# Optimization experiments

Measured on AMD Instinct MI355X. Metric: run time of the kernel, lower is better.

The kernel has to match this reference:

```python
import jax, jax.numpy as jnp
import numpy as np

B, L, D, H, HD = 4, 2048, 1024, 16, 64
SCALE = 1.0 / np.sqrt(HD)
NEG_INF = -1e9


def _apply_rope(x, rope):
    # x: (B, H, L, HD), rope: (L, HD)
    sin = rope[:, ::2]   # (L, HD/2)
    cos = rope[:, 1::2]  # (L, HD/2)
    x_even = x[..., ::2]
    x_odd = x[..., 1::2]
    r_even = x_even * cos - x_odd * sin
    r_odd = x_even * sin + x_odd * cos
    # interleave even/odd back: stack on new last axis then flatten
    return jnp.stack([r_even, r_odd], axis=-1).reshape(x.shape)


def setup_inputs() -> dict:
    key = jax.random.key(0)
    ks = jax.random.split(key, 10)
    s = 0.02
    inp = {
        "q_in": jax.random.normal(ks[0], (B, L, D), jnp.float32),
        "k_in": jax.random.normal(ks[1], (B, L, D), jnp.float32),
        "v_in": jax.random.normal(ks[2], (B, L, D), jnp.float32),
        "mask": jnp.broadcast_to(jnp.tril(jnp.ones((L, L), bool)), (B, L, L)),
        "rope": jax.random.normal(ks[3], (L, HD), jnp.float32),
        "Wq": jax.random.normal(ks[4], (D, H * HD), jnp.float32) * s,
        "bq": jnp.zeros((H * HD,), jnp.float32),
        "Wkv": jax.random.normal(ks[5], (D, 2 * H * HD), jnp.float32) * s,
        "bkv": jnp.zeros((2 * H * HD,), jnp.float32),
        "Wp": jax.random.normal(ks[6], (H * HD, D), jnp.float32) * s,
        "bp": jnp.zeros((D,), jnp.float32),
    }
    return inp


def reference(q_in, k_in, v_in, mask, rope, Wq, bq, Wkv, bkv, Wp, bp):
    q = q_in @ Wq + bq                       # (B, Lq, H*HD)
    kv = k_in @ Wkv + bkv                    # (B, Lk, 2*H*HD)
    k, v = jnp.split(kv, 2, axis=-1)
    q = q.reshape(B, L, H, HD).transpose(0, 2, 1, 3)  # (B, H, Lq, HD)
    k = k.reshape(B, L, H, HD).transpose(0, 2, 1, 3)
    v = v.reshape(B, L, H, HD).transpose(0, 2, 1, 3)
    # rope.shape[0] == Lq == Lk, so both branches fire
    q = _apply_rope(q, rope)
    k = _apply_rope(k, rope)
    logits = jnp.einsum("bhqd,bhkd->bhqk", q, k) * SCALE
    logits = jnp.where(mask[:, None, :, :], logits, NEG_INF)
    attn = jax.nn.softmax(logits, axis=-1)
    out = jnp.einsum("bhqk,bhkd->bhqd", attn, v)
    out = out.transpose(0, 2, 1, 3).reshape(B, L, H * HD)
    return out @ Wp + bp
```

## Files before the change

### kernel.cpp

```cpp
#include <hip/hip_runtime.h>
#include <hip/hip_bf16.h>

typedef __hip_bfloat16 bf16;
typedef short s16x8 __attribute__((ext_vector_type(8)));
typedef float f32x4 __attribute__((ext_vector_type(4)));

#define MFMA16(a, b, c) __builtin_amdgcn_mfma_f32_16x16x32_bf16(a, b, c, 0, 0, 0)
#define SCALE 0.125f

typedef __attribute__((address_space(1))) void gvoid;
typedef __attribute__((address_space(3))) void lvoid;

static __device__ __forceinline__ void lds_cp16(const bf16* g, bf16* l) {
    __builtin_amdgcn_global_load_lds((gvoid*)g, (lvoid*)l, 16, 0, 0);
}

static __device__ __forceinline__ void cast8(const float* __restrict__ src,
                                             bf16* __restrict__ dst, int i) {
    float4 a = *(const float4*)(src + i);
    float4 b = *(const float4*)(src + i + 4);
    bf16 o[8];
    o[0] = __float2bfloat16(a.x); o[1] = __float2bfloat16(a.y);
    o[2] = __float2bfloat16(a.z); o[3] = __float2bfloat16(a.w);
    o[4] = __float2bfloat16(b.x); o[5] = __float2bfloat16(b.y);
    o[6] = __float2bfloat16(b.z); o[7] = __float2bfloat16(b.w);
    *(uint4*)(dst + i) = *(const uint4*)o;
}

__global__ __launch_bounds__(256) void prep(
    const float* __restrict__ q_in, bf16* __restrict__ qbf,
    const float* __restrict__ k_in, bf16* __restrict__ kbf,
    const float* __restrict__ rope, bf16* __restrict__ ropec,
    const float* __restrict__ bq, const float* __restrict__ bkv,
    const float* __restrict__ bp, bf16* __restrict__ bqc,
    bf16* __restrict__ bkvc, bf16* __restrict__ bpc,
    const float* __restrict__ Wq, bf16* __restrict__ WqT,
    const float* __restrict__ Wkv, bf16* __restrict__ WkvT,
    const float* __restrict__ Wp, bf16* __restrict__ WpT) {
    __shared__ bf16 t[32][33];
    const int blk = blockIdx.x;
    const int tid = threadIdx.x;
    if (blk < 8192) {
        int i = (blk * 256 + tid) * 8;
        const float* src;
        bf16* dst;
        if (i < 8388608) {
            src = q_in; dst = qbf;
        } else {
            src = k_in; dst = kbf; i -= 8388608;
        }
        cast8(src, dst, i);
    } else if (blk < 12288) {
        int t2 = blk - 8192;
        int bx = t2 & 127;
        const int y = t2 >> 7;
        const float* in;
        bf16* out;
        int C;
        if (bx < 32) {
            in = Wq; out = WqT; C = 1024;
        } else if (bx < 96) {
            in = Wkv; out = WkvT; C = 2048; bx -= 32;
        } else {
            in = Wp; out = WpT; C = 1024; bx -= 96;
        }
        const int tx = tid & 31, ty = tid >> 5;
        const int c0 = bx * 32, r0 = y * 32;
        for (int i = ty; i < 32; i += 8)
            t[i][tx] = __float2bfloat16(in[(size_t)(r0 + i) * C + c0 + tx]);
        __syncthreads();
        for (int i = ty; i < 32; i += 8)
            out[(size_t)(c0 + i) * 1024 + r0 + tx] = t[tx][i];
    } else if (blk < 12352) {
        int i = ((blk - 12288) * 256 + tid) * 8;
        cast8(rope, ropec, i);
    } else {
        int i = ((blk - 12352) * 256 + tid) * 8;
        const float* src;
        bf16* dst;
        int off;
        if (i < 1024) {
            src = bq; dst = bqc; off = i;
        } else if (i < 3072) {
            src = bkv; dst = bkvc; off = i - 1024;
        } else {
            src = bp; dst = bpc; off = i - 3072;
        }
        cast8(src, dst, off);
    }
}

template <int EPI, int ROPE>
__device__ __forceinline__ void gemm_core(
    const bf16* __restrict__ A, const bf16* __restrict__ BT,
    const bf16* __restrict__ bias, const bf16* __restrict__ ropetab,
    void* __restrict__ out0, bf16* __restrict__ out1, int N, int K, int bx,
    int by, bf16* smA, bf16* smB) {
    const int tid = threadIdx.x;
    const int lane = tid & 63;
    const int wave = tid >> 6;
    const int lm = lane & 15;
    const int lq = lane >> 4;
    const int bm0 = by * 128;
    const int bn0 = bx * 128;
    const int wm = (wave >> 1) * 64;
    const int wn = (wave & 1) * 64;
    const int x7 = lm & 7;

    int srow[4], scol[4], sdst[4];
#pragma unroll
    for (int j = 0; j < 4; ++j) {
        int o = (wave * 4 + j) * 1024 + lane * 16;
        srow[j] = o >> 7;
        scol[j] = (((o >> 4) & 7) ^ (srow[j] & 7)) * 8;
        sdst[j] = (wave * 4 + j) * 512;
    }

    const f32x4 z4 = {0.f, 0.f, 0.f, 0.f};
    f32x4 acc[4][4];
#pragma unroll
    for (int i = 0; i < 4; ++i)
#pragma unroll
        for (int j = 0; j < 4; ++j) acc[i][j] = z4;

    const bf16* gA = A + (size_t)bm0 * K;
    const bf16* gB = BT + (size_t)bn0 * K;
    const int nk = K >> 6;
    for (int kt = 0; kt < nk; ++kt) {
        const size_t ko = (size_t)kt * 64;
#pragma unroll
        for (int j = 0; j < 4; ++j) {
            lds_cp16(gA + (size_t)srow[j] * K + ko + scol[j], smA + sdst[j]);
            lds_cp16(gB + (size_t)srow[j] * K + ko + scol[j], smB + sdst[j]);
        }
        __syncthreads();

#pragma unroll
        for (int kk = 0; kk < 2; ++kk) {
            s16x8 af[4], bfr[4];
#pragma unroll
            for (int i = 0; i < 4; ++i) {
                const int c16 = kk * 4 + lq;
                af[i] = *(const s16x8*)(smA + (wm + i * 16 + lm) * 64 +
                                        ((c16 ^ x7) * 8));
                bfr[i] = *(const s16x8*)(smB + (wn + i * 16 + lm) * 64 +
                                         ((c16 ^ x7) * 8));
            }
            __builtin_amdgcn_s_setprio(1);
#pragma unroll
            for (int i = 0; i < 4; ++i)
#pragma unroll
                for (int j = 0; j < 4; ++j)
                    acc[i][j] = MFMA16(af[i], bfr[j], acc[i][j]);
            __builtin_amdgcn_s_setprio(0);
        }
        __syncthreads();
    }

    if (EPI == 2 && bn0 >= 1024) {
        bf16* T = smA;
#pragma unroll
        for (int j = 0; j < 4; ++j) {
            const int nl = wn + j * 16 + lm;
            const float bv = __bfloat162float(bias[bn0 + nl]);
            const int xsw = (nl & 7) << 3;
#pragma unroll
            for (int i = 0; i < 4; ++i) {
                const int m0 = wm + i * 16 + lq * 4;
                bf16 pk[4];
#pragma unroll
                for (int r = 0; r < 4; ++r)
                    pk[r] = __float2bfloat16(acc[i][j][r] + bv);
                *(uint2*)(T + nl * 128 + (m0 ^ xsw)) = *(const uint2*)pk;
            }
        }
        __syncthreads();
        const int b = bm0 >> 11;
        const int lbase = bm0 & 2047;
#pragma unroll
        for (int p = 0; p < 8; ++p) {
            const int task = p * 256 + tid;
            const int row = task >> 4;
            const int chunk = task & 15;
            const int m8 = chunk * 8;
            uint4 v = *(const uint4*)(T + row * 128 + (m8 ^ ((row & 7) << 3)));
            const int n2 = bn0 - 1024 + row;
            const int h = n2 >> 6, hd = n2 & 63;
            *(uint4*)(out1 + (((size_t)(b * 16 + h) * 64) + hd) * 2048 +
                      lbase + m8) = v;
        }
        return;
    }

#pragma unroll
    for (int j = 0; j < 4; ++j) {
        const int n = bn0 + wn + j * 16 + lm;
        const float bv = __bfloat162float(bias[n]);
#pragma unroll
        for (int i = 0; i < 4; ++i) {
#pragma unroll
            for (int r = 0; r < 4; ++r) {
                const int m = bm0 + wm + i * 16 + lq * 4 + r;
                float v = acc[i][j][r] + bv;
                if (EPI == 0) {
                    ((float*)out0)[(size_t)m * N + n] = v;
                } else {
                    const int b = m >> 11, l = m & 2047;
                    if (ROPE) {
                        float w = __shfl_xor(v, 1, 64);
                        unsigned sc =
                            ((const unsigned*)ropetab)[l * 32 + ((n & 63) >> 1)];
                        float sn = __uint_as_float(sc << 16);
                        float cs = __uint_as_float(sc & 0xffff0000u);
                        v = (n & 1) ? (w * sn + v * cs) : (v * cs - w * sn);
                    }
                    const int h = (n & 1023) >> 6, hd = n & 63;
                    ((bf16*)out0)[(((size_t)(b * 16 + h) * 2048) + l) * 64 +
                                  hd] = __float2bfloat16(v);
                }
            }
        }
    }
}

__global__ __launch_bounds__(256) void gemm_qk(
    const bf16* __restrict__ qbf, const bf16* __restrict__ WqT,
    const bf16* __restrict__ bqc, const bf16* __restrict__ kbf,
    const bf16* __restrict__ WkvT, const bf16* __restrict__ bkvc,
    const bf16* __restrict__ ropec, bf16* __restrict__ qw,
    bf16* __restrict__ kw, bf16* __restrict__ vtw) {
    __shared__ __align__(16) bf16 sm[2 * 128 * 64];
    const int lid = blockIdx.x + 24 * blockIdx.y;
    const int xcd = lid & 7;
    const int slot = lid >> 3;
    const int by = xcd * 8 + (slot & 7);
    const int bx = slot >> 3;
    if (bx < 8)
        gemm_core<1, 1>(qbf, WqT, bqc, ropec, qw, (bf16*)nullptr, 1024, 1024,
                        bx, by, sm, sm + 8192);
    else
        gemm_core<2, 1>(kbf, WkvT, bkvc, ropec, kw, vtw, 2048, 1024, bx - 8,
                        by, sm, sm + 8192);
}

__global__ __launch_bounds__(256) void gemm_out(const bf16* __restrict__ A,
                                                const bf16* __restrict__ WpT,
                                                const bf16* __restrict__ bpc,
                                                float* __restrict__ out) {
    __shared__ __align__(16) bf16 sm[2 * 128 * 64];
    const int lid = blockIdx.x + 8 * blockIdx.y;
    const int xcd = lid & 7;
    const int slot = lid >> 3;
    const int by = xcd * 8 + (slot & 7);
    const int bx = slot >> 3;
    gemm_core<0, 0>(A, WpT, bpc, (const bf16*)nullptr, out, (bf16*)nullptr,
                    1024, 1024, bx, by, sm, sm + 8192);
}

__global__ __launch_bounds__(256, 4) void attn_causal(
    const bf16* __restrict__ Q, const bf16* __restrict__ Kc,
    const bf16* __restrict__ VT, bf16* __restrict__ O) {
    __shared__ __align__(16) bf16 smK[64 * 64];
    __shared__ __align__(16) bf16 smV[64 * 64];
    __shared__ __align__(16) bf16 p_lds[4][2][16 * 40];

    const int tid = threadIdx.x;
    const int lane = tid & 63;
    const int wave = tid >> 6;
    const int lm = lane & 15;
    const int lq = lane >> 4;
    const int x7 = lm & 7;
    const int bh = blockIdx.x;
    const int ya = (int)blockIdx.y >> 2, yb = (int)blockIdx.y & 3;
    const int base4 = (ya == 0) ? 15 : (ya == 1) ? 8 : (ya == 2) ? 7 : 0;
    const int pj = base4 + ((ya & 1) ? yb : -yb);
    const int qblk = pj * 128;
    const int q0 = qblk + wave * 16;
    const int nt = (qblk >> 6) + 2;
    const int b = bh >> 4, h = bh & 15;
    const int q0u = __builtin_amdgcn_readfirstlane(q0);

    const bf16* kp = Kc + (size_t)bh * 2048 * 64;
    const bf16* vp = VT + (size_t)bh * 64 * 2048;
    bf16* plA = &p_lds[wave][0][0];
    bf16* plB = &p_lds[wave][1][0];
    const f32x4 z4 = {0.f, 0.f, 0.f, 0.f};

    int srow[2], scol[2], sdst[2];
#pragma unroll
    for (int j = 0; j < 2; ++j) {
        int o = (wave * 2 + j) * 1024 + lane * 16;
        srow[j] = o >> 7;
        scol[j] = (((o >> 4) & 7) ^ (srow[j] & 7)) * 8;
        sdst[j] = (wave * 2 + j) * 512;
    }

    const bf16* qp = Q + ((size_t)bh * 2048 + q0) * 64;
    s16x8 aq0 = *(const s16x8*)(qp + lm * 64 + lq * 8);
    s16x8 aq1 = *(const s16x8*)(qp + lm * 64 + 32 + lq * 8);
    s16x8 aq2 = *(const s16x8*)(qp + 64 * 64 + lm * 64 + lq * 8);
    s16x8 aq3 = *(const s16x8*)(qp + 64 * 64 + lm * 64 + 32 + lq * 8);

    f32x4 o0[4], o1[4];
#pragma unroll
    for (int c = 0; c < 4; ++c) { o0[c] = z4; o1[c] = z4; }
    float ls0[4] = {0.f, 0.f, 0.f, 0.f};
    float ls1[4] = {0.f, 0.f, 0.f, 0.f};

#define ATTEND_SET(AQ0, AQ1, OO, LS, ROWBASE, ROWU)                           \
    {                                                                         \
        s16x8 kf[8];                                                          \
        _Pragma("unroll") for (int i = 0; i < 8; ++i) {                       \
            const int key = lm + (i >> 1) * 16;                               \
            const int c16 = (i & 1) * 4 + lq;                                 \
            kf[i] = *(const s16x8*)(smK + key * 64 + ((c16 ^ x7) * 8));       \
        }                                                                     \
        __builtin_amdgcn_s_setprio(1);                                        \
        f32x4 sA0 = z4, sA1 = z4, sB0 = z4, sB1 = z4;                         \
        sA0 = MFMA16(AQ0, kf[0], sA0);                                        \
        sA0 = MFMA16(AQ1, kf[1], sA0);                                        \
        sA1 = MFMA16(AQ0, kf[2], sA1);                                        \
        sA1 = MFMA16(AQ1, kf[3], sA1);                                        \
        sB0 = MFMA16(AQ0, kf[4], sB0);                                        \
        sB0 = MFMA16(AQ1, kf[5], sB0);                                        \
        sB1 = MFMA16(AQ0, kf[6], sB1);                                        \
        sB1 = MFMA16(AQ1, kf[7], sB1);                                        \
        __builtin_amdgcn_s_setprio(0);                                        \
        if (kb + 63 <= (ROWU)) {                                              \
            _Pragma("unroll") for (int r = 0; r < 4; ++r) {                   \
                float pA0 = __expf(sA0[r] * SCALE);                           \
                float pA1 = __expf(sA1[r] * SCALE);                           \
                float pB0 = __expf(sB0[r] * SCALE);                           \
                float pB1 = __expf(sB1[r] * SCALE);                           \
                LS[r] += (pA0 + pA1) + (pB0 + pB1);                           \
                plA[(lq * 4 + r) * 40 + lm] = __float2bfloat16(pA0);          \
                plA[(lq * 4 + r) * 40 + 16 + lm] = __float2bfloat16(pA1);     \
                plB[(lq * 4 + r) * 40 + lm] = __float2bfloat16(pB0);          \
                plB[(lq * 4 + r) * 40 + 16 + lm] = __float2bfloat16(pB1);     \
            }                                                                 \
        } else {                                                              \
            _Pragma("unroll") for (int r = 0; r < 4; ++r) {                   \
                const int rowg = (ROWBASE) + lq * 4 + r;                      \
                float pA0 = (kb + lm <= rowg) ? __expf(sA0[r] * SCALE) : 0.f; \
                float pA1 =                                                   \
                    (kb + 16 + lm <= rowg) ? __expf(sA1[r] * SCALE) : 0.f;    \
                float pB0 =                                                   \
                    (kb + 32 + lm <= rowg) ? __expf(sB0[r] * SCALE) : 0.f;    \
                float pB1 =                                                   \
                    (kb + 48 + lm <= rowg) ? __expf(sB1[r] * SCALE) : 0.f;    \
                LS[r] += (pA0 + pA1) + (pB0 + pB1);                           \
                plA[(lq * 4 + r) * 40 + lm] = __float2bfloat16(pA0);          \
                plA[(lq * 4 + r) * 40 + 16 + lm] = __float2bfloat16(pA1);     \
                plB[(lq * 4 + r) * 40 + lm] = __float2bfloat16(pB0);          \
                plB[(lq * 4 + r) * 40 + 16 + lm] = __float2bfloat16(pB1);     \
            }                                                                 \
        }                                                                     \
        s16x8 paA = *(const s16x8*)(plA + lm * 40 + lq * 8);                  \
        s16x8 paB = *(const s16x8*)(plB + lm * 40 + lq * 8);                  \
        __builtin_amdgcn_s_setprio(1);                                        \
        _Pragma("unroll") for (int c = 0; c < 4; ++c) {                       \
            const int hd = c * 16 + lm;                                       \
            s16x8 bvA = *(const s16x8*)(smV + hd * 64 + ((lq ^ x7) * 8));     \
            s16x8 bvB =                                                       \
                *(const s16x8*)(smV + hd * 64 + (((lq + 4) ^ x7) * 8));       \
            OO[c] = MFMA16(paA, bvA, OO[c]);                                  \
            OO[c] = MFMA16(paB, bvB, OO[c]);                                  \
        }                                                                     \
        __builtin_amdgcn_s_setprio(0);                                        \
    }

#pragma unroll
    for (int j = 0; j < 2; ++j) {
        lds_cp16(kp + (size_t)srow[j] * 64 + scol[j], smK + sdst[j]);
        lds_cp16(vp + (size_t)srow[j] * 2048 + scol[j], smV + sdst[j]);
    }
    __syncthreads();

    for (int it = 0; it < nt; ++it) {
        const int kb = it * 64;
        const bool more = (it + 1 < nt);

        uint4 kreg[2], vreg[2];
        if (more) {
            const int kn = kb + 64;
#pragma unroll
            for (int j = 0; j < 2; ++j) {
                kreg[j] = *(const uint4*)(kp + (size_t)(kn + srow[j]) * 64 +
                                          scol[j]);
                vreg[j] = *(const uint4*)(vp + (size_t)srow[j] * 2048 + kn +
                                          scol[j]);
            }
        }

        if (it < nt - 1) {
            ATTEND_SET(aq0, aq1, o0, ls0, q0, q0u);
        }
        ATTEND_SET(aq2, aq3, o1, ls1, q0 + 64, q0u + 64);

        if (more) {
            __syncthreads();
#pragma unroll
            for (int j = 0; j < 2; ++j) {
                *(uint4*)(smK + sdst[j] + lane * 8) = kreg[j];
                *(uint4*)(smV + sdst[j] + lane * 8) = vreg[j];
            }
            __syncthreads();
        }
    }
#undef ATTEND_SET

#pragma unroll
    for (int r = 0; r < 4; ++r) {
        float s = ls0[r];
        s += __shfl_xor(s, 1, 64);
        s += __shfl_xor(s, 2, 64);
        s += __shfl_xor(s, 4, 64);
        s += __shfl_xor(s, 8, 64);
        ls0[r] = s;
        float t = ls1[r];
        t += __shfl_xor(t, 1, 64);
        t += __shfl_xor(t, 2, 64);
        t += __shfl_xor(t, 4, 64);
        t += __shfl_xor(t, 8, 64);
        ls1[r] = t;
    }

#pragma unroll
    for (int c = 0; c < 4; ++c) {
#pragma unroll
        for (int r = 0; r < 4; ++r) {
            const int hd = c * 16 + lm;
            const int l0 = q0 + lq * 4 + r;
            O[((size_t)(b * 2048 + l0)) * 1024 + h * 64 + hd] =
                __float2bfloat16(o0[c][r] / ls0[r]);
            const int l1 = l0 + 64;
            O[((size_t)(b * 2048 + l1)) * 1024 + h * 64 + hd] =
                __float2bfloat16(o1[c][r] / ls1[r]);
        }
    }
}

extern "C" void kernel_launch(void* const* d_in, const int* in_sizes, int n_in,
                              void* d_out, int out_size, void* d_ws,
                              size_t ws_size, hipStream_t stream) {
    const float* q_in = (const float*)d_in[0];
    const float* k_in = (const float*)d_in[1];
    const float* rope = (const float*)d_in[4];
    const float* Wq = (const float*)d_in[5];
    const float* bq = (const float*)d_in[6];
    const float* Wkv = (const float*)d_in[7];
    const float* bkv = (const float*)d_in[8];
    const float* Wp = (const float*)d_in[9];
    const float* bp = (const float*)d_in[10];
    float* out = (float*)d_out;

    char* ws = (char*)d_ws;
    bf16* bqc = (bf16*)ws;   ws += 2048;
    bf16* bkvc = (bf16*)ws;  ws += 4096;
    bf16* bpc = (bf16*)ws;   ws += 2048;
    bf16* ropec = (bf16*)ws; ws += 262144;
    bf16* WqT = (bf16*)ws;   ws += 2097152;
    bf16* WkvT = (bf16*)ws;  ws += 4194304;
    bf16* WpT = (bf16*)ws;   ws += 2097152;
    bf16* qw = (bf16*)ws;    ws += 16777216;
    bf16* kw = (bf16*)ws;    ws += 16777216;
    bf16* vtw = (bf16*)ws;   ws += 16777216;
    bf16* aw = (bf16*)ws;    ws += 16777216;
    bf16* qbf = aw;
    bf16* kbf = (bf16*)d_out;

    dim3 blk(256);

    prep<<<12354, blk, 0, stream>>>(q_in, qbf, k_in, kbf, rope, ropec, bq, bkv,
                                    bp, bqc, bkvc, bpc, Wq, WqT, Wkv, WkvT, Wp,
                                    WpT);

    gemm_qk<<<dim3(24, 64), blk, 0, stream>>>(qbf, WqT, bqc, kbf, WkvT, bkvc,
                                              ropec, qw, kw, vtw);

    attn_causal<<<dim3(64, 16), blk, 0, stream>>>(qw, kw, vtw, aw);

    gemm_out<<<dim3(8, 64), blk, 0, stream>>>(aw, WpT, bpc, out);
}
```

Before: 221.4 us.

## Double-buffer K/V tiles in LDS with async global-to-LDS loads in attention

Result: faster. 177.6 us (median of 2 runs) (-19.8%).

```diff
diff --git a/kernel.cpp b/kernel.cpp
--- a/kernel.cpp
+++ b/kernel.cpp
@@ -257,11 +257,11 @@
                     1024, 1024, bx, by, sm, sm + 8192);
 }
 
-__global__ __launch_bounds__(256, 4) void attn_causal(
+__global__ __launch_bounds__(256, 3) void attn_causal(
     const bf16* __restrict__ Q, const bf16* __restrict__ Kc,
     const bf16* __restrict__ VT, bf16* __restrict__ O) {
-    __shared__ __align__(16) bf16 smK[64 * 64];
-    __shared__ __align__(16) bf16 smV[64 * 64];
+    __shared__ __align__(16) bf16 smK[2][64 * 64];
+    __shared__ __align__(16) bf16 smV[2][64 * 64];
     __shared__ __align__(16) bf16 p_lds[4][2][16 * 40];
 
     const int tid = threadIdx.x;
@@ -313,7 +313,7 @@
         _Pragma("unroll") for (int i = 0; i < 8; ++i) {                       \
             const int key = lm + (i >> 1) * 16;                               \
             const int c16 = (i & 1) * 4 + lq;                                 \
-            kf[i] = *(const s16x8*)(smK + key * 64 + ((c16 ^ x7) * 8));       \
+            kf[i] = *(const s16x8*)(sK + key * 64 + ((c16 ^ x7) * 8));        \
         }                                                                     \
         __builtin_amdgcn_s_setprio(1);                                        \
         f32x4 sA0 = z4, sA1 = z4, sB0 = z4, sB1 = z4;                         \
@@ -360,9 +360,9 @@
         __builtin_amdgcn_s_setprio(1);                                        \
         _Pragma("unroll") for (int c = 0; c < 4; ++c) {                       \
             const int hd = c * 16 + lm;                                       \
-            s16x8 bvA = *(const s16x8*)(smV + hd * 64 + ((lq ^ x7) * 8));     \
+            s16x8 bvA = *(const s16x8*)(sV + hd * 64 + ((lq ^ x7) * 8));      \
             s16x8 bvB =                                                       \
-                *(const s16x8*)(smV + hd * 64 + (((lq + 4) ^ x7) * 8));       \
+                *(const s16x8*)(sV + hd * 64 + (((lq + 4) ^ x7) * 8));        \
             OO[c] = MFMA16(paA, bvA, OO[c]);                                  \
             OO[c] = MFMA16(paB, bvB, OO[c]);                                  \
         }                                                                     \
@@ -371,26 +371,31 @@
 
 #pragma unroll
     for (int j = 0; j < 2; ++j) {
-        lds_cp16(kp + (size_t)srow[j] * 64 + scol[j], smK + sdst[j]);
-        lds_cp16(vp + (size_t)srow[j] * 2048 + scol[j], smV + sdst[j]);
+        lds_cp16(kp + (size_t)srow[j] * 64 + scol[j], &smK[0][0] + sdst[j]);
+        lds_cp16(vp + (size_t)srow[j] * 2048 + scol[j], &smV[0][0] + sdst[j]);
     }
     __syncthreads();
 
+    int cur = 0;
     for (int it = 0; it < nt; ++it) {
         const int kb = it * 64;
         const bool more = (it + 1 < nt);
 
-        uint4 kreg[2], vreg[2];
         if (more) {
             const int kn = kb + 64;
+            bf16* dK = &smK[cur ^ 1][0];
+            bf16* dV = &smV[cur ^ 1][0];
 #pragma unroll
             for (int j = 0; j < 2; ++j) {
-                kreg[j] = *(const uint4*)(kp + (size_t)(kn + srow[j]) * 64 +
-                                          scol[j]);
-                vreg[j] = *(const uint4*)(vp + (size_t)srow[j] * 2048 + kn +
-                                          scol[j]);
+                lds_cp16(kp + (size_t)(kn + srow[j]) * 64 + scol[j],
+                         dK + sdst[j]);
+                lds_cp16(vp + (size_t)srow[j] * 2048 + kn + scol[j],
+                         dV + sdst[j]);
             }
         }
+
+        const bf16* sK = &smK[cur][0];
+        const bf16* sV = &smV[cur][0];
 
         if (it < nt - 1) {
             ATTEND_SET(aq0, aq1, o0, ls0, q0, q0u);
@@ -399,12 +404,7 @@
 
         if (more) {
             __syncthreads();
-#pragma unroll
-            for (int j = 0; j < 2; ++j) {
-                *(uint4*)(smK + sdst[j] + lane * 8) = kreg[j];
-                *(uint4*)(smV + sdst[j] + lane * 8) = vreg[j];
-            }
-            __syncthreads();
+            cur ^= 1;
         }
     }
 #undef ATTEND_SET
```
